# Performance work log

Measured on AMD Instinct MI355X. Metric: run time of the kernel, lower is better.

## Reference

```python
import jax, jax.numpy as jnp
import numpy as np

ROPE_BASE = 10000.0
NUM_HEADS = 16
NUM_KV_HEADS = 4


def _rms_norm(x, eps):
    # F.rms_norm with no weight: x / sqrt(mean(x^2) + eps)
    return x * jax.lax.rsqrt(jnp.mean(x * x, axis=-1, keepdims=True) + eps)


def _apply_rope(x, cos, sin):
    h = x.shape[-1] // 2
    x1, x2 = x[..., :h], x[..., h:]
    return jnp.concatenate([x1 * cos + x2 * sin, -x1 * sin + x2 * cos], axis=-1)


def setup_inputs() -> dict:
    key = jax.random.key(0)
    ks = jax.random.split(key, 5)
    B, T, D = 2, 2048, 1024
    H, Hkv = NUM_HEADS, NUM_KV_HEADS
    hd = D // H
    kv_dim = Hkv * hd
    s_in = 1.0 / np.sqrt(D)
    return {
        "x": jax.random.normal(ks[0], (B, T, D), dtype=jnp.float32),
        "Wq": jax.random.normal(ks[1], (D, D), dtype=jnp.float32) * s_in,
        "Wk": jax.random.normal(ks[2], (kv_dim, D), dtype=jnp.float32) * s_in,
        "Wv": jax.random.normal(ks[3], (kv_dim, D), dtype=jnp.float32) * s_in,
        "Wproj": jax.random.normal(ks[4], (D, D), dtype=jnp.float32) * s_in,
        "q_gain": jnp.full((H,), 1.0, dtype=jnp.float32),
    }


def reference(x, Wq, Wk, Wv, Wproj, q_gain):
    B, T, D = x.shape
    H, Hkv = NUM_HEADS, NUM_KV_HEADS
    hd = D // H
    rep = H // Hkv
    eps = jnp.finfo(x.dtype).eps

    # QKV projections (F.linear: x @ W.T)
    q = jnp.einsum('btd,od->bto', x, Wq).reshape(B, T, H, hd).transpose(0, 2, 1, 3)
    k = jnp.einsum('btd,od->bto', x, Wk).reshape(B, T, Hkv, hd).transpose(0, 2, 1, 3)
    v = jnp.einsum('btd,od->bto', x, Wv).reshape(B, T, Hkv, hd).transpose(0, 2, 1, 3)

    q = _rms_norm(q, eps)
    k = _rms_norm(k, eps)

    # RoPE tables: [1, 1, T, hd/2]
    inv_freq = 1.0 / (ROPE_BASE ** (jnp.arange(0, hd, 2, dtype=jnp.float32) / hd))
    f = jnp.arange(T, dtype=jnp.float32)[:, None] * inv_freq[None, :]
    cos = jnp.cos(f)[None, None].astype(q.dtype)
    sin = jnp.sin(f)[None, None].astype(q.dtype)
    q = _apply_rope(q, cos, sin)
    k = _apply_rope(k, cos, sin)

    q = q * q_gain.astype(q.dtype)[None, :, None, None]

    # GQA without materializing repeated K/V: group q heads [Hkv, rep]
    qg = q.reshape(B, Hkv, rep, T, hd)
    scale = hd ** -0.5
    scores = jnp.einsum('bgrqd,bgkd->bgrqk', qg, k) * scale
    causal = jnp.tril(jnp.ones((T, T), dtype=bool))
    scores = jnp.where(causal, scores, -jnp.inf)
    att = jax.nn.softmax(scores.astype(jnp.float32), axis=-1).astype(q.dtype)
    y = jnp.einsum('bgrqk,bgkd->bgrqd', att, v)  # [B,Hkv,rep,T,hd]
    y = y.reshape(B, H, T, hd).transpose(0, 2, 1, 3).reshape(B, T, D)
    return jnp.einsum('btd,od->bto', y, Wproj)
```

## Files before the change

### kernel.cpp

```cpp
#include <hip/hip_runtime.h>
#include <cstdint>
#include <cstddef>

typedef __attribute__((ext_vector_type(8))) short short8;
typedef __attribute__((ext_vector_type(4))) float floatx4;
typedef __attribute__((ext_vector_type(16))) float floatx16;
typedef __attribute__((ext_vector_type(4))) short short4v;
typedef unsigned short u16;
typedef unsigned int u32;

#define B_   2
#define T_   2048
#define D_   1024
#define H_   16
#define HKV_ 4
#define HD_  64
#define KV_  256
#define M_   4096
#define QS_  1536

#define NX   4194304
#define NWQ  1048576
#define NWK  262144
#define NWV  262144
#define NWP  1048576
#define NCAST (NX + NWQ + NWK + NWV + NWP)
#define CAST_BLOCKS (NCAST / 1024)
#define TAB_BLOCKS  256

__device__ __forceinline__ float b2f(u16 u) {
    union { u32 i; float f; } v; v.i = ((u32)u) << 16; return v.f;
}
__device__ __forceinline__ u16 f2b(float f) {
    union { float f; u32 i; } v; v.f = f;
    u32 r = v.i + 0x7FFF + ((v.i >> 16) & 1);
    return (u16)(r >> 16);
}

__device__ __forceinline__ void async16(const u16* g, u16* l) {
    __builtin_amdgcn_global_load_lds(
        (const __attribute__((address_space(1))) u32*)g,
        (__attribute__((address_space(3))) u32*)l, 16, 0, 0);
}

__device__ __forceinline__ u32 cvtpk(float lo, float hi) {
    u32 r;
    asm("v_cvt_pk_bf16_f32 %0, %1, %2" : "=v"(r) : "v"(lo), "v"(hi));
    return r;
}
__device__ __forceinline__ void swap32(u32& a, u32& b) {
    asm volatile("v_permlane32_swap_b32 %0, %1" : "+v"(a), "+v"(b));
}
__device__ __forceinline__ void swap32f(float& a, float& b) {
    asm volatile("v_permlane32_swap_b32 %0, %1" : "+v"(a), "+v"(b));
}
__device__ __forceinline__ short8 pkfrag(u32 w0, u32 w1, u32 w2, u32 w3) {
    union { u32 w[4]; short8 s; } u;
    u.w[0] = w0; u.w[1] = w1; u.w[2] = w2; u.w[3] = w3;
    return u.s;
}

__global__ __launch_bounds__(256) void prep(const float* __restrict__ x,
                                            const float* __restrict__ wq,
                                            const float* __restrict__ wk,
                                            const float* __restrict__ wv,
                                            const float* __restrict__ wp,
                                            u16* __restrict__ dst,
                                            float2* __restrict__ tab) {
    int blk = blockIdx.x;
    if (blk < CAST_BLOCKS) {
        int i = blk * 1024 + threadIdx.x * 4;
        const float* src; int off;
        if      (i < NX)                  { src = x;  off = i; }
        else if (i < NX+NWQ)              { src = wq; off = i - NX; }
        else if (i < NX+NWQ+NWK)          { src = wk; off = i - (NX+NWQ); }
        else if (i < NX+NWQ+NWK+NWV)      { src = wv; off = i - (NX+NWQ+NWK); }
        else                              { src = wp; off = i - (NX+NWQ+NWK+NWV); }
        float4 v = *(const float4*)(src + off);
        short4v o;
        o.x = (short)f2b(v.x); o.y = (short)f2b(v.y);
        o.z = (short)f2b(v.z); o.w = (short)f2b(v.w);
        *(short4v*)(dst + i) = o;
    } else {
        int idx = (blk - CAST_BLOCKS) * 256 + threadIdx.x;
        int t = idx >> 5, i = idx & 31;
        float freq = exp2f(-(float)i * (13.287712379549449f / 32.0f));
        float ang = (float)t * freq;
        tab[idx] = make_float2(cosf(ang), sinf(ang));
    }
}

__global__ __launch_bounds__(256, 3) void gemm_qkv(const u16* __restrict__ A,
                                                   const u16* __restrict__ W,
                                                   u16* __restrict__ C,
                                                   u16* __restrict__ Vt,
                                                   const float* __restrict__ gain,
                                                   const float2* __restrict__ tab) {
    const int K = D_;
    __shared__ u16 As[2][2][128 * 32];
    __shared__ u16 Bs[2][2][64 * 32];
    const int t = threadIdx.x;
    const int wave = t >> 6, lane = t & 63;
    const int quad = lane >> 4, l16 = lane & 15;
    const int wm = wave * 32;
    const int m0 = blockIdx.y * 128, n0 = blockIdx.x * 64;

    floatx4 acc[2][4];
#pragma unroll
    for (int i = 0; i < 2; i++)
#pragma unroll
        for (int j = 0; j < 4; j++) acc[i][j] = (floatx4){0.f, 0.f, 0.f, 0.f};

    const int sr = t >> 2;
    const int sc = (((t & 3) ^ ((t >> 3) & 3)) * 8);
    const u16* ga = A + (size_t)(m0 + sr) * K + sc;
    const u16* gb = W + (size_t)(n0 + sr) * K + sc;

    auto stage = [&](int buf, int half, int koff) {
        async16(ga + koff, As[buf][half] + t * 8);
        async16(ga + koff + (size_t)64 * K, As[buf][half] + t * 8 + 64 * 32);
        async16(gb + koff, Bs[buf][half] + t * 8);
    };

    stage(0, 0, 0);
    stage(0, 1, 32);

    int cur = 0;
    for (int kt = 0; kt < K; kt += 64) {
        __syncthreads();
        if (kt + 64 < K) {
            stage(cur ^ 1, 0, kt + 64);
            stage(cur ^ 1, 1, kt + 96);
        }
#pragma unroll
        for (int half = 0; half < 2; half++) {
            short8 af[2], bf[4];
#pragma unroll
            for (int mt = 0; mt < 2; mt++) {
                int row = wm + mt * 16 + l16;
                af[mt] = *(const short8*)(As[cur][half] + row * 32 +
                                          ((quad ^ ((row >> 1) & 3)) << 3));
            }
#pragma unroll
            for (int nt = 0; nt < 4; nt++) {
                int row = nt * 16 + l16;
                bf[nt] = *(const short8*)(Bs[cur][half] + row * 32 +
                                          ((quad ^ ((row >> 1) & 3)) << 3));
            }
#pragma unroll
            for (int mt = 0; mt < 2; mt++)
#pragma unroll
                for (int nt = 0; nt < 4; nt++)
                    acc[mt][nt] = __builtin_amdgcn_mfma_f32_16x16x32_bf16(
                        af[mt], bf[nt], acc[mt][nt], 0, 0, 0);
        }
        cur ^= 1;
    }

    const int col0 = n0;
    if (col0 < 1280) {
        float gs = (col0 < 1024)
                 ? gain[col0 >> 6] * (0.125f * 1.4426950408889634f)
                 : 1.0f;
#pragma unroll
        for (int mt = 0; mt < 2; mt++)
#pragma unroll
            for (int r = 0; r < 4; r++) {
                int row = m0 + wm + mt * 16 + quad * 4 + r;
                int tt = row & (T_ - 1);
                float v0 = acc[mt][0][r], v1 = acc[mt][1][r];
                float v2 = acc[mt][2][r], v3 = acc[mt][3][r];
                float ss = v0 * v0 + v1 * v1 + v2 * v2 + v3 * v3;
                ss += __shfl_xor(ss, 1); ss += __shfl_xor(ss, 2);
                ss += __shfl_xor(ss, 4); ss += __shfl_xor(ss, 8);
                float inv = rsqrtf(ss * (1.0f / 64.0f) + 1.1920929e-7f);
                v0 *= inv; v1 *= inv; v2 *= inv; v3 *= inv;
                float2 cs0 = tab[tt * 32 + l16];
                float2 cs1 = tab[tt * 32 + 16 + l16];
                float o0 = (v0 * cs0.x + v2 * cs0.y) * gs;
                float o1 = (v1 * cs1.x + v3 * cs1.y) * gs;
                float o2 = (v2 * cs0.x - v0 * cs0.y) * gs;
                float o3 = (v3 * cs1.x - v1 * cs1.y) * gs;
                u16* cp = C + (size_t)row * QS_ + col0 + l16;
                cp[0]  = f2b(o0);
                cp[16] = f2b(o1);
                cp[32] = f2b(o2);
                cp[48] = f2b(o3);
            }
    } else {
        const int g = (col0 - 1280) >> 6;
#pragma unroll
        for (int mt = 0; mt < 2; mt++)
#pragma unroll
            for (int r = 0; r < 4; r++) {
                int row = m0 + wm + mt * 16 + quad * 4 + r;
                int tt = row & (T_ - 1);
                int bb = row >> 11;
#pragma unroll
                for (int nt = 0; nt < 4; nt++)
                    Vt[(size_t)((bb * 4 + g) * 64 + nt * 16 + l16) * T_ + tt] =
                        f2b(acc[mt][nt][r]);
            }
    }
}

__global__ __launch_bounds__(256, 3) void gemm_proj(const u16* __restrict__ A,
                                                    const u16* __restrict__ W,
                                                    float* __restrict__ C) {
    const int K = D_;
    __shared__ u16 As[2][2][128 * 32];
    __shared__ u16 Bs[2][2][64 * 32];
    const int t = threadIdx.x;
    const int wave = t >> 6, lane = t & 63;
    const int quad = lane >> 4, l16 = lane & 15;
    const int wm = wave * 32;
    const int m0 = blockIdx.y * 128, n0 = blockIdx.x * 64;

    floatx4 acc[2][4];
#pragma unroll
    for (int i = 0; i < 2; i++)
#pragma unroll
        for (int j = 0; j < 4; j++) acc[i][j] = (floatx4){0.f, 0.f, 0.f, 0.f};

    const int sr = t >> 2;
    const int sc = (((t & 3) ^ ((t >> 3) & 3)) * 8);
    const u16* ga = A + (size_t)(m0 + sr) * K + sc;
    const u16* gb = W + (size_t)(n0 + sr) * K + sc;

    auto stage = [&](int buf, int half, int koff) {
        async16(ga + koff, As[buf][half] + t * 8);
        async16(ga + koff + (size_t)64 * K, As[buf][half] + t * 8 + 64 * 32);
        async16(gb + koff, Bs[buf][half] + t * 8);
    };

    stage(0, 0, 0);
    stage(0, 1, 32);

    int cur = 0;
    for (int kt = 0; kt < K; kt += 64) {
        __syncthreads();
        if (kt + 64 < K) {
            stage(cur ^ 1, 0, kt + 64);
            stage(cur ^ 1, 1, kt + 96);
        }
#pragma unroll
        for (int half = 0; half < 2; half++) {
            short8 af[2], bf[4];
#pragma unroll
            for (int mt = 0; mt < 2; mt++) {
                int row = wm + mt * 16 + l16;
                af[mt] = *(const short8*)(As[cur][half] + row * 32 +
                                          ((quad ^ ((row >> 1) & 3)) << 3));
            }
#pragma unroll
            for (int nt = 0; nt < 4; nt++) {
                int row = nt * 16 + l16;
                bf[nt] = *(const short8*)(Bs[cur][half] + row * 32 +
                                          ((quad ^ ((row >> 1) & 3)) << 3));
            }
#pragma unroll
            for (int mt = 0; mt < 2; mt++)
#pragma unroll
                for (int nt = 0; nt < 4; nt++)
                    acc[mt][nt] = __builtin_amdgcn_mfma_f32_16x16x32_bf16(
                        af[mt], bf[nt], acc[mt][nt], 0, 0, 0);
        }
        cur ^= 1;
    }

#pragma unroll
    for (int mt = 0; mt < 2; mt++)
#pragma unroll
        for (int nt = 0; nt < 4; nt++)
#pragma unroll
            for (int r = 0; r < 4; r++) {
                int row = m0 + wm + mt * 16 + quad * 4 + r;
                int col = n0 + nt * 16 + l16;
                C[(size_t)row * D_ + col] = acc[mt][nt][r];
            }
}

__global__ __launch_bounds__(256, 2) void flash(const u16* __restrict__ QKV,
                                                const u16* __restrict__ Vtr,
                                                u16* __restrict__ Y,
                                                float* __restrict__ Opart,
                                                float* __restrict__ Lpart) {
    const int u  = blockIdx.x;
    const int h  = blockIdx.y;
    const int b  = blockIdx.z;
    const int g  = h >> 2;
    const int w    = threadIdx.x >> 6;
    const int lane = threadIdx.x & 63;
    const int ln31 = lane & 31;
    const int hi   = lane >> 5;
    const int swz  = lane & 7;

    __shared__ u16 Kb[3][4096];
    __shared__ u16 Vb[3][4096];
    __shared__ float Ot[4][2048];

    const int srow = w * 16 + (lane >> 3);
    const int sseg = (lane & 7) ^ ((lane >> 3) & 7);
    const u16* kgb = QKV + (size_t)(b * T_ + srow) * QS_ + D_ + g * 64 + sseg * 8;
    const u16* vgb = Vtr + (size_t)((b * 4 + g) * 64 + srow) * T_ + sseg * 8;

    auto stage = [&](int tile, int bi) {
        const u16* kg = kgb + (size_t)tile * 64 * QS_;
        const u16* vg = vgb + (size_t)tile * 64;
        u16* kl = &Kb[bi][w * 1024 + lane * 8];
        u16* vl = &Vb[bi][w * 1024 + lane * 8];
        async16(kg, kl);
        async16(kg + (size_t)8 * QS_, kl + 512);
        async16(vg, vl);
        async16(vg + (size_t)8 * T_, vl + 512);
    };
    const bool low = (u < 8);
    auto tileOf = [&](int gidx) {
        return (low && gidx > 2 * u + 1) ? gidx + 15 - 2 * u : gidx;
    };

    stage(tileOf(0), 0);
    stage(tileOf(1), 1);

    const int nseg = low ? 2 : 1;
    const int buf  = low ? 0 : 1;
    int gi = 0;
    for (int seg = 0; seg < nseg; ++seg) {
        const int jt   = (low && seg == 0) ? u : (low ? 15 - u : u);
        const int nIt  = (low && seg == 0) ? 2 * u + 2 : (low ? 15 - 2 * u : 17);
        const bool direct = low && (seg == 0);
        const int qrow = jt * 128 + w * 32 + ln31;

        const u16* qp = QKV + (size_t)(b * T_ + qrow) * QS_ + h * HD_;
        short8 aq[4];
#pragma unroll
        for (int kc = 0; kc < 4; kc++)
            aq[kc] = *(const short8*)(qp + kc * 16 + hi * 8);

        floatx16 acc[2];
#pragma unroll
        for (int dh = 0; dh < 2; dh++)
#pragma unroll
            for (int i = 0; i < 16; i++) acc[dh][i] = 0.f;
        float l = 0.f;

        for (int itn = 0; itn < nIt; ++itn, ++gi) {
            const int tk = tileOf(gi);
            if (gi == 16) asm volatile("s_waitcnt vmcnt(0)" ::: "memory");
            else          asm volatile("s_waitcnt vmcnt(4)" ::: "memory");
            __builtin_amdgcn_s_barrier();
            asm volatile("" ::: "memory");

            const int bc = gi % 3;
            if (gi + 2 <= 16) stage(tileOf(gi + 2), (gi + 2) % 3);

            const u16* Kp = &Kb[bc][0];
            const u16* Vp = &Vb[bc][0];
            short8 kf[2][4], vfr[2][4];
#pragma unroll
            for (int kh = 0; kh < 2; kh++)
#pragma unroll
                for (int kc = 0; kc < 4; kc++)
                    kf[kh][kc] = *(const short8*)(Kp + (kh * 32 + ln31) * 64 +
                                                  (((kc * 2 + hi) ^ swz) << 3));
#pragma unroll
            for (int dh = 0; dh < 2; dh++)
#pragma unroll
                for (int kc = 0; kc < 4; kc++)
                    vfr[dh][kc] = *(const short8*)(Vp + (dh * 32 + ln31) * 64 +
                                                   (((kc * 2 + hi) ^ swz) << 3));

            floatx16 s[2];
#pragma unroll
            for (int kh = 0; kh < 2; kh++)
#pragma unroll
                for (int i = 0; i < 16; i++) s[kh][i] = 0.f;

            __builtin_amdgcn_s_setprio(1);
#pragma unroll
            for (int kc = 0; kc < 4; kc++) {
                s[0] = __builtin_amdgcn_mfma_f32_32x32x16_bf16(kf[0][kc], aq[kc], s[0], 0, 0, 0);
                s[1] = __builtin_amdgcn_mfma_f32_32x32x16_bf16(kf[1][kc], aq[kc], s[1], 0, 0, 0);
            }
            __builtin_amdgcn_s_setprio(0);

            u32 pw[2][8];
            if (tk >= 2 * jt) {
#pragma unroll
                for (int kh = 0; kh < 2; kh++)
#pragma unroll
                    for (int i = 0; i < 8; i++) {
                        int key0 = tk * 64 + kh * 32 +
                                   ((2 * i) & 3) + (((2 * i) >> 2) << 3) + (hi << 2);
                        float e0 = __builtin_amdgcn_exp2f(s[kh][2 * i]);
                        float e1 = __builtin_amdgcn_exp2f(s[kh][2 * i + 1]);
                        e0 = (key0 <= qrow) ? e0 : 0.f;
                        e1 = (key0 + 1 <= qrow) ? e1 : 0.f;
                        l += e0 + e1;
                        pw[kh][i] = cvtpk(e0, e1);
                    }
            } else {
#pragma unroll
                for (int kh = 0; kh < 2; kh++)
#pragma unroll
                    for (int i = 0; i < 8; i++) {
                        float e0 = __builtin_amdgcn_exp2f(s[kh][2 * i]);
                        float e1 = __builtin_amdgcn_exp2f(s[kh][2 * i + 1]);
                        l += e0 + e1;
                        pw[kh][i] = cvtpk(e0, e1);
                    }
            }

            short8 pb[4];
#pragma unroll
            for (int kh = 0; kh < 2; kh++) {
                u32 a0 = pw[kh][0], b0 = pw[kh][2], c0 = pw[kh][1], d0 = pw[kh][3];
                swap32(a0, b0); swap32(c0, d0);
                pb[kh * 2] = pkfrag(a0, c0, b0, d0);
                u32 a1 = pw[kh][4], b1 = pw[kh][6], c1 = pw[kh][5], d1 = pw[kh][7];
                swap32(a1, b1); swap32(c1, d1);
                pb[kh * 2 + 1] = pkfrag(a1, c1, b1, d1);
            }

            __builtin_amdgcn_s_setprio(1);
#pragma unroll
            for (int kc = 0; kc < 4; kc++) {
                acc[0] = __builtin_amdgcn_mfma_f32_32x32x16_bf16(vfr[0][kc], pb[kc], acc[0], 0, 0, 0);
                acc[1] = __builtin_amdgcn_mfma_f32_32x32x16_bf16(vfr[1][kc], pb[kc], acc[1], 0, 0, 0);
            }
            __builtin_amdgcn_s_setprio(0);
        }

        float la = l, lb = l;
        swap32f(la, lb);
        float lt = la + lb;

        if (direct) {
            float inv = 1.0f / lt;
#pragma unroll
            for (int dh = 0; dh < 2; dh++)
#pragma unroll
                for (int i = 0; i < 16; i++) acc[dh][i] *= inv;
        }

        float* ot = &Ot[w][0];
#pragma unroll
        for (int dh = 0; dh < 2; dh++)
#pragma unroll
            for (int g4 = 0; g4 < 4; g4++) {
                int ss = (dh * 8 + g4 * 2 + hi) ^ (ln31 & 7);
                float4 v = make_float4(acc[dh][g4 * 4 + 0], acc[dh][g4 * 4 + 1],
                                       acc[dh][g4 * 4 + 2], acc[dh][g4 * 4 + 3]);
                *(float4*)(ot + ln31 * 64 + ss * 4) = v;
            }
        asm volatile("s_waitcnt lgkmcnt(0)" ::: "memory");

        const int hq = lane >> 4;
        const int s4 = lane & 15;
        if (direct) {
            u16* ybase = Y + (size_t)(b * T_ + jt * 128 + w * 32) * D_ + h * HD_;
#pragma unroll
            for (int it = 0; it < 8; it++) {
                int q2 = it * 4 + hq;
                int ss = s4 ^ (q2 & 7);
                float4 v = *(const float4*)(ot + q2 * 64 + ss * 4);
                uint2 yw;
                yw.x = cvtpk(v.x, v.y);
                yw.y = cvtpk(v.z, v.w);
                *(uint2*)(ybase + (size_t)q2 * D_ + s4 * 4) = yw;
            }
        } else {
            const int rp = jt * 128 + w * 32 - 1024;
            float* obase = Opart + ((size_t)((buf * 2 + b) * 1024 + rp)) * 1024
                         + h * HD_;
#pragma unroll
            for (int it = 0; it < 8; it++) {
                int q2 = it * 4 + hq;
                int ss = s4 ^ (q2 & 7);
                float4 v = *(const float4*)(ot + q2 * 64 + ss * 4);
                *(float4*)(obase + (size_t)q2 * 1024 + s4 * 4) = v;
            }
            if (hi == 0)
                Lpart[((size_t)((buf * 2 + b) * 1024 + rp + ln31)) * 16 + h] = lt;
        }
    }
}

__global__ __launch_bounds__(256) void combine(const float* __restrict__ Opart,
                                               const float* __restrict__ Lpart,
                                               u16* __restrict__ Y) {
    int e = (blockIdx.x * 256 + threadIdx.x) * 4;
    int b = e >> 20;
    int rem = e & 1048575;
    int row = rem >> 10, col = rem & 1023;
    int li = (b * 1024 + row) * 16 + (col >> 6);
    float l0 = Lpart[li];
    float l1 = Lpart[li + 2 * 1024 * 16];
    float inv = 1.0f / (l0 + l1);
    size_t oi = ((size_t)(b * 1024 + row)) * 1024 + col;
    float4 o0 = *(const float4*)(Opart + oi);
    float4 o1 = *(const float4*)(Opart + oi + (size_t)2 * 1024 * 1024);
    short4v y;
    y.x = (short)f2b((o0.x + o1.x) * inv); y.y = (short)f2b((o0.y + o1.y) * inv);
    y.z = (short)f2b((o0.z + o1.z) * inv); y.w = (short)f2b((o0.w + o1.w) * inv);
    *(short4v*)(Y + (size_t)(b * T_ + 1024 + row) * D_ + col) = y;
}

extern "C" void kernel_launch(void* const* d_in, const int* in_sizes, int n_in,
                              void* d_out, int out_size, void* d_ws, size_t ws_size,
                              hipStream_t stream) {
    const float* x    = (const float*)d_in[0];
    const float* Wq   = (const float*)d_in[1];
    const float* Wk   = (const float*)d_in[2];
    const float* Wv   = (const float*)d_in[3];
    const float* Wp   = (const float*)d_in[4];
    const float* gain = (const float*)d_in[5];
    float* out = (float*)d_out;

    u16* xb   = (u16*)d_ws;
    u16* Wcat = xb + (size_t)NX;
    u16* Wpb  = Wcat + (size_t)(NWQ + NWK + NWV);
    u16* QKV  = Wpb + (size_t)NWP;
    u16* Vt   = QKV + (size_t)M_ * QS_;
    u16* Y    = Vt + (size_t)M_ * KV_;
    float2* tab = (float2*)(Y + (size_t)M_ * D_);
    float* Opart = (float*)(tab + 65536);
    float* Lpart = Opart + (size_t)4 * 1024 * 1024;

    prep<<<CAST_BLOCKS + TAB_BLOCKS, 256, 0, stream>>>(x, Wq, Wk, Wv, Wp, xb, tab);

    gemm_qkv<<<dim3(QS_ / 64, M_ / 128), 256, 0, stream>>>(xb, Wcat, QKV, Vt,
                                                           gain, tab);

    flash<<<dim3(16, H_, B_), 256, 0, stream>>>(QKV, Vt, Y, Opart, Lpart);

    combine<<<2048, 256, 0, stream>>>(Opart, Lpart, Y);

    gemm_proj<<<dim3(D_ / 64, M_ / 128), 256, 0, stream>>>(Y, Wpb, out);
}
```

Baseline: 160.4 us.

## Split flash warps 2x2 over query and key halves with LDS reduction

Restructures the flash kernel's warp work split. Each pair of warps now shares 64 query rows, and each warp handles one 32-key half of the K tile and one half of the V reduction dimension, instead of every warp owning 32 query rows against all 64 keys. This halves the K and V LDS fragment reads per warp and reuses each K fragment across two query blocks. In exchange it adds a cross-warp LDS reduction of the partial O and l, reusing a free V buffer for l, plus two extra barriers per segment, and it keeps more accumulator registers live.

```diff
diff --git a/kernel.cpp b/kernel.cpp
--- a/kernel.cpp
+++ b/kernel.cpp
@@ -294,10 +294,12 @@
     const int ln31 = lane & 31;
     const int hi   = lane >> 5;
     const int swz  = lane & 7;
+    const int qw   = w >> 1;
+    const int kw   = w & 1;
 
     __shared__ u16 Kb[3][4096];
     __shared__ u16 Vb[3][4096];
-    __shared__ float Ot[4][2048];
+    __shared__ float Ot[8192];
 
     const int srow = w * 16 + (lane >> 3);
     const int sseg = (lane & 7) ^ ((lane >> 3) & 7);
@@ -329,20 +331,25 @@
         const int jt   = (low && seg == 0) ? u : (low ? 15 - u : u);
         const int nIt  = (low && seg == 0) ? 2 * u + 2 : (low ? 15 - 2 * u : 17);
         const bool direct = low && (seg == 0);
-        const int qrow = jt * 128 + w * 32 + ln31;
-
-        const u16* qp = QKV + (size_t)(b * T_ + qrow) * QS_ + h * HD_;
-        short8 aq[4];
-#pragma unroll
-        for (int kc = 0; kc < 4; kc++)
-            aq[kc] = *(const short8*)(qp + kc * 16 + hi * 8);
-
-        floatx16 acc[2];
+        const int qbase = jt * 128 + qw * 64;
+
+        const u16* qp = QKV + (size_t)(b * T_ + qbase + ln31) * QS_ + h * HD_;
+        short8 aq[2][4];
+#pragma unroll
+        for (int qh = 0; qh < 2; qh++)
+#pragma unroll
+            for (int kc = 0; kc < 4; kc++)
+                aq[qh][kc] = *(const short8*)(qp + (size_t)qh * 32 * QS_ +
+                                              kc * 16 + hi * 8);
+
+        floatx16 acc[2][2];
 #pragma unroll
         for (int dh = 0; dh < 2; dh++)
 #pragma unroll
-            for (int i = 0; i < 16; i++) acc[dh][i] = 0.f;
-        float l = 0.f;
+            for (int qh = 0; qh < 2; qh++)
+#pragma unroll
+                for (int i = 0; i < 16; i++) acc[dh][qh][i] = 0.f;
+        float l[2] = {0.f, 0.f};
 
         for (int itn = 0; itn < nIt; ++itn, ++gi) {
             const int tk = tileOf(gi);
@@ -356,132 +363,201 @@
 
             const u16* Kp = &Kb[bc][0];
             const u16* Vp = &Vb[bc][0];
-            short8 kf[2][4], vfr[2][4];
-#pragma unroll
-            for (int kh = 0; kh < 2; kh++)
-#pragma unroll
-                for (int kc = 0; kc < 4; kc++)
-                    kf[kh][kc] = *(const short8*)(Kp + (kh * 32 + ln31) * 64 +
-                                                  (((kc * 2 + hi) ^ swz) << 3));
+
+            short8 kf[4];
+#pragma unroll
+            for (int kc = 0; kc < 4; kc++)
+                kf[kc] = *(const short8*)(Kp + (kw * 32 + ln31) * 64 +
+                                          (((kc * 2 + hi) ^ swz) << 3));
+
+            floatx16 s2[2];
+#pragma unroll
+            for (int qh = 0; qh < 2; qh++)
+#pragma unroll
+                for (int i = 0; i < 16; i++) s2[qh][i] = 0.f;
+
+            __builtin_amdgcn_s_setprio(1);
+#pragma unroll
+            for (int kc = 0; kc < 4; kc++) {
+                s2[0] = __builtin_amdgcn_mfma_f32_32x32x16_bf16(kf[kc], aq[0][kc], s2[0], 0, 0, 0);
+                s2[1] = __builtin_amdgcn_mfma_f32_32x32x16_bf16(kf[kc], aq[1][kc], s2[1], 0, 0, 0);
+            }
+            __builtin_amdgcn_s_setprio(0);
+
+            short8 vfr[2][2];
 #pragma unroll
             for (int dh = 0; dh < 2; dh++)
 #pragma unroll
-                for (int kc = 0; kc < 4; kc++)
-                    vfr[dh][kc] = *(const short8*)(Vp + (dh * 32 + ln31) * 64 +
-                                                   (((kc * 2 + hi) ^ swz) << 3));
-
-            floatx16 s[2];
-#pragma unroll
-            for (int kh = 0; kh < 2; kh++)
-#pragma unroll
-                for (int i = 0; i < 16; i++) s[kh][i] = 0.f;
-
-            __builtin_amdgcn_s_setprio(1);
-#pragma unroll
-            for (int kc = 0; kc < 4; kc++) {
-                s[0] = __builtin_amdgcn_mfma_f32_32x32x16_bf16(kf[0][kc], aq[kc], s[0], 0, 0, 0);
-                s[1] = __builtin_amdgcn_mfma_f32_32x32x16_bf16(kf[1][kc], aq[kc], s[1], 0, 0, 0);
-            }
-            __builtin_amdgcn_s_setprio(0);
-
-            u32 pw[2][8];
-            if (tk >= 2 * jt) {
-#pragma unroll
-                for (int kh = 0; kh < 2; kh++)
+                for (int kc2 = 0; kc2 < 2; kc2++)
+                    vfr[dh][kc2] = *(const short8*)(Vp + (dh * 32 + ln31) * 64 +
+                                        (((kw * 4 + kc2 * 2 + hi) ^ swz) << 3));
+
+            short8 pb[2][2];
+#pragma unroll
+            for (int qh = 0; qh < 2; qh++) {
+                const int qrow = qbase + qh * 32 + ln31;
+                u32 pw[8];
+                if (tk >= 2 * jt) {
 #pragma unroll
                     for (int i = 0; i < 8; i++) {
-                        int key0 = tk * 64 + kh * 32 +
+                        int key0 = tk * 64 + kw * 32 +
                                    ((2 * i) & 3) + (((2 * i) >> 2) << 3) + (hi << 2);
-                        float e0 = __builtin_amdgcn_exp2f(s[kh][2 * i]);
-                        float e1 = __builtin_amdgcn_exp2f(s[kh][2 * i + 1]);
+                        float e0 = __builtin_amdgcn_exp2f(s2[qh][2 * i]);
+                        float e1 = __builtin_amdgcn_exp2f(s2[qh][2 * i + 1]);
                         e0 = (key0 <= qrow) ? e0 : 0.f;
                         e1 = (key0 + 1 <= qrow) ? e1 : 0.f;
-                        l += e0 + e1;
-                        pw[kh][i] = cvtpk(e0, e1);
+                        l[qh] += e0 + e1;
+                        pw[i] = cvtpk(e0, e1);
                     }
-            } else {
-#pragma unroll
-                for (int kh = 0; kh < 2; kh++)
+                } else {
 #pragma unroll
                     for (int i = 0; i < 8; i++) {
-                        float e0 = __builtin_amdgcn_exp2f(s[kh][2 * i]);
-                        float e1 = __builtin_amdgcn_exp2f(s[kh][2 * i + 1]);
-                        l += e0 + e1;
-                        pw[kh][i] = cvtpk(e0, e1);
+                        float e0 = __builtin_amdgcn_exp2f(s2[qh][2 * i]);
+                        float e1 = __builtin_amdgcn_exp2f(s2[qh][2 * i + 1]);
+                        l[qh] += e0 + e1;
+                        pw[i] = cvtpk(e0, e1);
                     }
-            }
-
-            short8 pb[4];
-#pragma unroll
-            for (int kh = 0; kh < 2; kh++) {
-                u32 a0 = pw[kh][0], b0 = pw[kh][2], c0 = pw[kh][1], d0 = pw[kh][3];
+                }
+                u32 a0 = pw[0], c0 = pw[1], b0 = pw[2], d0 = pw[3];
                 swap32(a0, b0); swap32(c0, d0);
-                pb[kh * 2] = pkfrag(a0, c0, b0, d0);
-                u32 a1 = pw[kh][4], b1 = pw[kh][6], c1 = pw[kh][5], d1 = pw[kh][7];
+                pb[qh][0] = pkfrag(a0, c0, b0, d0);
+                u32 a1 = pw[4], c1 = pw[5], b1 = pw[6], d1 = pw[7];
                 swap32(a1, b1); swap32(c1, d1);
-                pb[kh * 2 + 1] = pkfrag(a1, c1, b1, d1);
+                pb[qh][1] = pkfrag(a1, c1, b1, d1);
             }
 
             __builtin_amdgcn_s_setprio(1);
 #pragma unroll
-            for (int kc = 0; kc < 4; kc++) {
-                acc[0] = __builtin_amdgcn_mfma_f32_32x32x16_bf16(vfr[0][kc], pb[kc], acc[0], 0, 0, 0);
-                acc[1] = __builtin_amdgcn_mfma_f32_32x32x16_bf16(vfr[1][kc], pb[kc], acc[1], 0, 0, 0);
+            for (int kc2 = 0; kc2 < 2; kc2++) {
+                acc[0][0] = __builtin_amdgcn_mfma_f32_32x32x16_bf16(vfr[0][kc2], pb[0][kc2], acc[0][0], 0, 0, 0);
+                acc[0][1] = __builtin_amdgcn_mfma_f32_32x32x16_bf16(vfr[0][kc2], pb[1][kc2], acc[0][1], 0, 0, 0);
+                acc[1][0] = __builtin_amdgcn_mfma_f32_32x32x16_bf16(vfr[1][kc2], pb[0][kc2], acc[1][0], 0, 0, 0);
+                acc[1][1] = __builtin_amdgcn_mfma_f32_32x32x16_bf16(vfr[1][kc2], pb[1][kc2], acc[1][1], 0, 0, 0);
             }
             __builtin_amdgcn_s_setprio(0);
         }
 
-        float la = l, lb = l;
-        swap32f(la, lb);
-        float lt = la + lb;
-
-        if (direct) {
-            float inv = 1.0f / lt;
+        float lt[2];
+#pragma unroll
+        for (int qh = 0; qh < 2; qh++) {
+            float la = l[qh], lb = l[qh];
+            swap32f(la, lb);
+            lt[qh] = la + lb;
+        }
+
+        const int fb = (gi + 2) % 3;
+        float* Lsh = (float*)&Vb[fb][0];
+        float* otq = Ot + qw * 4096;
+
+        __builtin_amdgcn_s_barrier();
+        asm volatile("" ::: "memory");
+
+        if (kw == 1) {
 #pragma unroll
             for (int dh = 0; dh < 2; dh++)
 #pragma unroll
-                for (int i = 0; i < 16; i++) acc[dh][i] *= inv;
-        }
-
-        float* ot = &Ot[w][0];
-#pragma unroll
-        for (int dh = 0; dh < 2; dh++)
-#pragma unroll
-            for (int g4 = 0; g4 < 4; g4++) {
-                int ss = (dh * 8 + g4 * 2 + hi) ^ (ln31 & 7);
-                float4 v = make_float4(acc[dh][g4 * 4 + 0], acc[dh][g4 * 4 + 1],
-                                       acc[dh][g4 * 4 + 2], acc[dh][g4 * 4 + 3]);
-                *(float4*)(ot + ln31 * 64 + ss * 4) = v;
-            }
+                for (int qh = 0; qh < 2; qh++)
+#pragma unroll
+                    for (int g4 = 0; g4 < 4; g4++) {
+                        int ql = qh * 32 + ln31;
+                        int ss = (dh * 8 + g4 * 2 + hi) ^ (ln31 & 7);
+                        float4 v = make_float4(acc[dh][qh][g4 * 4 + 0],
+                                               acc[dh][qh][g4 * 4 + 1],
+                                               acc[dh][qh][g4 * 4 + 2],
+                                               acc[dh][qh][g4 * 4 + 3]);
+                        *(float4*)(otq + ql * 64 + ss * 4) = v;
+                    }
+            if (hi == 0) {
+                Lsh[(qw * 2 + 0) * 32 + ln31] = lt[0];
+                Lsh[(qw * 2 + 1) * 32 + ln31] = lt[1];
+            }
+        }
         asm volatile("s_waitcnt lgkmcnt(0)" ::: "memory");
+        __builtin_amdgcn_s_barrier();
+        asm volatile("" ::: "memory");
+
+        if (kw == 0) {
+            float ltot[2];
+#pragma unroll
+            for (int qh = 0; qh < 2; qh++)
+                ltot[qh] = lt[qh] + Lsh[(qw * 2 + qh) * 32 + ln31];
+#pragma unroll
+            for (int dh = 0; dh < 2; dh++)
+#pragma unroll
+                for (int qh = 0; qh < 2; qh++)
+#pragma unroll
+                    for (int g4 = 0; g4 < 4; g4++) {
+                        int ql = qh * 32 + ln31;
+                        int ss = (dh * 8 + g4 * 2 + hi) ^ (ln31 & 7);
+                        float4 v = *(const float4*)(otq + ql * 64 + ss * 4);
+                        acc[dh][qh][g4 * 4 + 0] += v.x;
+                        acc[dh][qh][g4 * 4 + 1] += v.y;
+                        acc[dh][qh][g4 * 4 + 2] += v.z;
+                        acc[dh][qh][g4 * 4 + 3] += v.w;
+                    }
+            if (direct) {
+#pragma unroll
+                for (int qh = 0; qh < 2; qh++) {
+                    float inv = 1.0f / ltot[qh];
+#pragma unroll
+                    for (int dh = 0; dh < 2; dh++)
+#pragma unroll
+                        for (int i = 0; i < 16; i++) acc[dh][qh][i] *= inv;
+                }
+            }
+#pragma unroll
+            for (int dh = 0; dh < 2; dh++)
+#pragma unroll
+                for (int qh = 0; qh < 2; qh++)
+#pragma unroll
+                    for (int g4 = 0; g4 < 4; g4++) {
+                        int ql = qh * 32 + ln31;
+                        int ss = (dh * 8 + g4 * 2 + hi) ^ (ln31 & 7);
+                        float4 v = make_float4(acc[dh][qh][g4 * 4 + 0],
+                                               acc[dh][qh][g4 * 4 + 1],
+                                               acc[dh][qh][g4 * 4 + 2],
+                                               acc[dh][qh][g4 * 4 + 3]);
+                        *(float4*)(otq + ql * 64 + ss * 4) = v;
+                    }
+            if (!direct && hi == 0) {
+                int rbase = (buf * 2 + b) * 1024 + jt * 128 - 1024 + qw * 64;
+                Lpart[(size_t)(rbase + ln31) * 16 + h] = ltot[0];
+                Lpart[(size_t)(rbase + 32 + ln31) * 16 + h] = ltot[1];
+            }
+        }
+        asm volatile("s_waitcnt lgkmcnt(0)" ::: "memory");
+        __builtin_amdgcn_s_barrier();
+        asm volatile("" ::: "memory");
 
         const int hq = lane >> 4;
         const int s4 = lane & 15;
         if (direct) {
-            u16* ybase = Y + (size_t)(b * T_ + jt * 128 + w * 32) * D_ + h * HD_;
+            u16* ybase = Y + (size_t)(b * T_ + jt * 128) * D_ + h * HD_;
 #pragma unroll
             for (int it = 0; it < 8; it++) {
                 int q2 = it * 4 + hq;
+                int q128 = w * 32 + q2;
                 int ss = s4 ^ (q2 & 7);
-                float4 v = *(const float4*)(ot + q2 * 64 + ss * 4);
+                float4 v = *(const float4*)(Ot + (q128 >> 6) * 4096 +
+                                            (q128 & 63) * 64 + ss * 4);
                 uint2 yw;
                 yw.x = cvtpk(v.x, v.y);
                 yw.y = cvtpk(v.z, v.w);
-                *(uint2*)(ybase + (size_t)q2 * D_ + s4 * 4) = yw;
+                *(uint2*)(ybase + (size_t)q128 * D_ + s4 * 4) = yw;
             }
         } else {
-            const int rp = jt * 128 + w * 32 - 1024;
+            const int rp = jt * 128 - 1024;
             float* obase = Opart + ((size_t)((buf * 2 + b) * 1024 + rp)) * 1024
                          + h * HD_;
 #pragma unroll
             for (int it = 0; it < 8; it++) {
                 int q2 = it * 4 + hq;
+                int q128 = w * 32 + q2;
                 int ss = s4 ^ (q2 & 7);
-                float4 v = *(const float4*)(ot + q2 * 64 + ss * 4);
-                *(float4*)(obase + (size_t)q2 * 1024 + s4 * 4) = v;
-            }
-            if (hi == 0)
-                Lpart[((size_t)((buf * 2 + b) * 1024 + rp + ln31)) * 16 + h] = lt;
+                float4 v = *(const float4*)(Ot + (q128 >> 6) * 4096 +
+                                            (q128 & 63) * 64 + ss * 4);
+                *(float4*)(obase + (size_t)q128 * 1024 + s4 * 4) = v;
+            }
         }
     }
 }
```

Measured after the change: 160.6 us. About the same (+0.1%).

## Split key tiles across wave pairs in flash and drop combine kernel

Applied to the files above, without the earlier changes.

Flash attention now runs 512-thread blocks where each pair of waves shares a 32-row query tile and splits each 64-key tile in half, reducing partial outputs through shared memory. Each block handles a paired low/high query tile with the full key range, so the split-K global partials and the separate combine kernel are removed. This cuts a kernel launch and the fp32 partial-output traffic, at the cost of half as many blocks, extra barriers and an in-block reduction.

```diff
diff --git a/kernel.cpp b/kernel.cpp
--- a/kernel.cpp
+++ b/kernel.cpp
@@ -280,56 +280,47 @@
             }
 }
 
-__global__ __launch_bounds__(256, 2) void flash(const u16* __restrict__ QKV,
+__global__ __launch_bounds__(512, 1) void flash(const u16* __restrict__ QKV,
                                                 const u16* __restrict__ Vtr,
-                                                u16* __restrict__ Y,
-                                                float* __restrict__ Opart,
-                                                float* __restrict__ Lpart) {
+                                                u16* __restrict__ Y) {
     const int u  = blockIdx.x;
     const int h  = blockIdx.y;
     const int b  = blockIdx.z;
     const int g  = h >> 2;
-    const int w    = threadIdx.x >> 6;
-    const int lane = threadIdx.x & 63;
+    const int t  = threadIdx.x;
+    const int w    = t >> 6;
+    const int lane = t & 63;
     const int ln31 = lane & 31;
     const int hi   = lane >> 5;
     const int swz  = lane & 7;
+    const int qw   = w >> 1;
+    const int kw   = w & 1;
 
     __shared__ u16 Kb[3][4096];
     __shared__ u16 Vb[3][4096];
-    __shared__ float Ot[4][2048];
-
-    const int srow = w * 16 + (lane >> 3);
-    const int sseg = (lane & 7) ^ ((lane >> 3) & 7);
+    __shared__ float Ot[8192];
+
+    const int srow = t >> 3;
+    const int sseg = (t & 7) ^ (srow & 7);
     const u16* kgb = QKV + (size_t)(b * T_ + srow) * QS_ + D_ + g * 64 + sseg * 8;
     const u16* vgb = Vtr + (size_t)((b * 4 + g) * 64 + srow) * T_ + sseg * 8;
 
     auto stage = [&](int tile, int bi) {
-        const u16* kg = kgb + (size_t)tile * 64 * QS_;
-        const u16* vg = vgb + (size_t)tile * 64;
-        u16* kl = &Kb[bi][w * 1024 + lane * 8];
-        u16* vl = &Vb[bi][w * 1024 + lane * 8];
-        async16(kg, kl);
-        async16(kg + (size_t)8 * QS_, kl + 512);
-        async16(vg, vl);
-        async16(vg + (size_t)8 * T_, vl + 512);
+        async16(kgb + (size_t)tile * 64 * QS_, &Kb[bi][t * 8]);
+        async16(vgb + (size_t)tile * 64,       &Vb[bi][t * 8]);
     };
-    const bool low = (u < 8);
-    auto tileOf = [&](int gidx) {
-        return (low && gidx > 2 * u + 1) ? gidx + 15 - 2 * u : gidx;
-    };
+    const int n0 = 2 * u + 2;
+    auto tileOf = [&](int gidx) { return (gidx < n0) ? gidx : gidx - n0; };
 
     stage(tileOf(0), 0);
     stage(tileOf(1), 1);
 
-    const int nseg = low ? 2 : 1;
-    const int buf  = low ? 0 : 1;
     int gi = 0;
-    for (int seg = 0; seg < nseg; ++seg) {
-        const int jt   = (low && seg == 0) ? u : (low ? 15 - u : u);
-        const int nIt  = (low && seg == 0) ? 2 * u + 2 : (low ? 15 - 2 * u : 17);
-        const bool direct = low && (seg == 0);
-        const int qrow = jt * 128 + w * 32 + ln31;
+    for (int seg = 0; seg < 2; ++seg) {
+        const int jt  = seg ? 15 - u : u;
+        const int nIt = seg ? 32 - 2 * u : 2 * u + 2;
+        const int qbase = jt * 128 + qw * 32;
+        const int qrow  = qbase + ln31;
 
         const u16* qp = QKV + (size_t)(b * T_ + qrow) * QS_ + h * HD_;
         short8 aq[4];
@@ -346,88 +337,76 @@
 
         for (int itn = 0; itn < nIt; ++itn, ++gi) {
             const int tk = tileOf(gi);
-            if (gi == 16) asm volatile("s_waitcnt vmcnt(0)" ::: "memory");
-            else          asm volatile("s_waitcnt vmcnt(4)" ::: "memory");
+            if (gi == 33) asm volatile("s_waitcnt vmcnt(0)" ::: "memory");
+            else          asm volatile("s_waitcnt vmcnt(2)" ::: "memory");
             __builtin_amdgcn_s_barrier();
             asm volatile("" ::: "memory");
 
             const int bc = gi % 3;
-            if (gi + 2 <= 16) stage(tileOf(gi + 2), (gi + 2) % 3);
+            if (gi + 2 <= 33) stage(tileOf(gi + 2), (gi + 2) % 3);
 
             const u16* Kp = &Kb[bc][0];
             const u16* Vp = &Vb[bc][0];
-            short8 kf[2][4], vfr[2][4];
-#pragma unroll
-            for (int kh = 0; kh < 2; kh++)
-#pragma unroll
-                for (int kc = 0; kc < 4; kc++)
-                    kf[kh][kc] = *(const short8*)(Kp + (kh * 32 + ln31) * 64 +
-                                                  (((kc * 2 + hi) ^ swz) << 3));
+
+            short8 kf[4];
+#pragma unroll
+            for (int kc = 0; kc < 4; kc++)
+                kf[kc] = *(const short8*)(Kp + (kw * 32 + ln31) * 64 +
+                                          (((kc * 2 + hi) ^ swz) << 3));
+
+            floatx16 s2;
+#pragma unroll
+            for (int i = 0; i < 16; i++) s2[i] = 0.f;
+
+            __builtin_amdgcn_s_setprio(1);
+#pragma unroll
+            for (int kc = 0; kc < 4; kc++)
+                s2 = __builtin_amdgcn_mfma_f32_32x32x16_bf16(kf[kc], aq[kc], s2, 0, 0, 0);
+            __builtin_amdgcn_s_setprio(0);
+
+            short8 vfr[2][2];
 #pragma unroll
             for (int dh = 0; dh < 2; dh++)
 #pragma unroll
-                for (int kc = 0; kc < 4; kc++)
-                    vfr[dh][kc] = *(const short8*)(Vp + (dh * 32 + ln31) * 64 +
-                                                   (((kc * 2 + hi) ^ swz) << 3));
-
-            floatx16 s[2];
-#pragma unroll
-            for (int kh = 0; kh < 2; kh++)
-#pragma unroll
-                for (int i = 0; i < 16; i++) s[kh][i] = 0.f;
+                for (int kc2 = 0; kc2 < 2; kc2++)
+                    vfr[dh][kc2] = *(const short8*)(Vp + (dh * 32 + ln31) * 64 +
+                                        (((kw * 4 + kc2 * 2 + hi) ^ swz) << 3));
+
+            u32 pw[8];
+            if (tk >= 2 * jt) {
+#pragma unroll
+                for (int i = 0; i < 8; i++) {
+                    int key0 = tk * 64 + kw * 32 +
+                               ((2 * i) & 3) + (((2 * i) >> 2) << 3) + (hi << 2);
+                    float e0 = __builtin_amdgcn_exp2f(s2[2 * i]);
+                    float e1 = __builtin_amdgcn_exp2f(s2[2 * i + 1]);
+                    e0 = (key0 <= qrow) ? e0 : 0.f;
+                    e1 = (key0 + 1 <= qrow) ? e1 : 0.f;
+                    l += e0 + e1;
+                    pw[i] = cvtpk(e0, e1);
+                }
+            } else {
+#pragma unroll
+                for (int i = 0; i < 8; i++) {
+                    float e0 = __builtin_amdgcn_exp2f(s2[2 * i]);
+                    float e1 = __builtin_amdgcn_exp2f(s2[2 * i + 1]);
+                    l += e0 + e1;
+                    pw[i] = cvtpk(e0, e1);
+                }
+            }
+
+            u32 a0 = pw[0], c0 = pw[1], b0 = pw[2], d0 = pw[3];
+            swap32(a0, b0); swap32(c0, d0);
+            short8 pb0 = pkfrag(a0, c0, b0, d0);
+            u32 a1 = pw[4], c1 = pw[5], b1 = pw[6], d1 = pw[7];
+            swap32(a1, b1); swap32(c1, d1);
+            short8 pb1 = pkfrag(a1, c1, b1, d1);
 
             __builtin_amdgcn_s_setprio(1);
-#pragma unroll
-            for (int kc = 0; kc < 4; kc++) {
-                s[0] = __builtin_amdgcn_mfma_f32_32x32x16_bf16(kf[0][kc], aq[kc], s[0], 0, 0, 0);
-                s[1] = __builtin_amdgcn_mfma_f32_32x32x16_bf16(kf[1][kc], aq[kc], s[1], 0, 0, 0);
-            }
-            __builtin_amdgcn_s_setprio(0);
-
-            u32 pw[2][8];
-            if (tk >= 2 * jt) {
-#pragma unroll
-                for (int kh = 0; kh < 2; kh++)
-#pragma unroll
-                    for (int i = 0; i < 8; i++) {
-                        int key0 = tk * 64 + kh * 32 +
-                                   ((2 * i) & 3) + (((2 * i) >> 2) << 3) + (hi << 2);
-                        float e0 = __builtin_amdgcn_exp2f(s[kh][2 * i]);
-                        float e1 = __builtin_amdgcn_exp2f(s[kh][2 * i + 1]);
-                        e0 = (key0 <= qrow) ? e0 : 0.f;
-                        e1 = (key0 + 1 <= qrow) ? e1 : 0.f;
-                        l += e0 + e1;
-                        pw[kh][i] = cvtpk(e0, e1);
-                    }
-            } else {
-#pragma unroll
-                for (int kh = 0; kh < 2; kh++)
-#pragma unroll
-                    for (int i = 0; i < 8; i++) {
-                        float e0 = __builtin_amdgcn_exp2f(s[kh][2 * i]);
-                        float e1 = __builtin_amdgcn_exp2f(s[kh][2 * i + 1]);
-                        l += e0 + e1;
-                        pw[kh][i] = cvtpk(e0, e1);
-                    }
-            }
-
-            short8 pb[4];
-#pragma unroll
-            for (int kh = 0; kh < 2; kh++) {
-                u32 a0 = pw[kh][0], b0 = pw[kh][2], c0 = pw[kh][1], d0 = pw[kh][3];
-                swap32(a0, b0); swap32(c0, d0);
-                pb[kh * 2] = pkfrag(a0, c0, b0, d0);
-                u32 a1 = pw[kh][4], b1 = pw[kh][6], c1 = pw[kh][5], d1 = pw[kh][7];
-                swap32(a1, b1); swap32(c1, d1);
-                pb[kh * 2 + 1] = pkfrag(a1, c1, b1, d1);
-            }
-
-            __builtin_amdgcn_s_setprio(1);
-#pragma unroll
-            for (int kc = 0; kc < 4; kc++) {
-                acc[0] = __builtin_amdgcn_mfma_f32_32x32x16_bf16(vfr[0][kc], pb[kc], acc[0], 0, 0, 0);
-                acc[1] = __builtin_amdgcn_mfma_f32_32x32x16_bf16(vfr[1][kc], pb[kc], acc[1], 0, 0, 0);
-            }
+            acc[0] = __builtin_amdgcn_mfma_f32_32x32x16_bf16(vfr[0][0], pb0, acc[0], 0, 0, 0);
+            acc[1] = __builtin_amdgcn_mfma_f32_32x32x16_bf16(vfr[1][0], pb0, acc[1], 0, 0, 0);
+            acc[0] = __builtin_amdgcn_mfma_f32_32x32x16_bf16(vfr[0][1], pb1, acc[0], 0, 0, 0);
+            acc[1] = __builtin_amdgcn_mfma_f32_32x32x16_bf16(vfr[1][1], pb1, acc[1], 0, 0, 0);
             __builtin_amdgcn_s_setprio(0);
         }
 
@@ -435,75 +414,67 @@
         swap32f(la, lb);
         float lt = la + lb;
 
-        if (direct) {
-            float inv = 1.0f / lt;
+        const int fb = (gi + 2) % 3;
+        float* Lsh = (float*)&Vb[fb][0];
+        float* otq = Ot + qw * 2048;
+
+        __builtin_amdgcn_s_barrier();
+        asm volatile("" ::: "memory");
+
+        if (kw == 1) {
 #pragma unroll
             for (int dh = 0; dh < 2; dh++)
 #pragma unroll
-                for (int i = 0; i < 16; i++) acc[dh][i] *= inv;
-        }
-
-        float* ot = &Ot[w][0];
-#pragma unroll
-        for (int dh = 0; dh < 2; dh++)
-#pragma unroll
-            for (int g4 = 0; g4 < 4; g4++) {
-                int ss = (dh * 8 + g4 * 2 + hi) ^ (ln31 & 7);
-                float4 v = make_float4(acc[dh][g4 * 4 + 0], acc[dh][g4 * 4 + 1],
-                                       acc[dh][g4 * 4 + 2], acc[dh][g4 * 4 + 3]);
-                *(float4*)(ot + ln31 * 64 + ss * 4) = v;
-            }
+                for (int g4 = 0; g4 < 4; g4++) {
+                    int ss = (dh * 8 + g4 * 2 + hi) ^ (ln31 & 7);
+                    float4 v = make_float4(acc[dh][g4 * 4 + 0],
+                                           acc[dh][g4 * 4 + 1],
+                                           acc[dh][g4 * 4 + 2],
+                                           acc[dh][g4 * 4 + 3]);
+                    *(float4*)(otq + ln31 * 64 + ss * 4) = v;
+                }
+            if (hi == 0) Lsh[qw * 32 + ln31] = lt;
+        }
         asm volatile("s_waitcnt lgkmcnt(0)" ::: "memory");
+        __builtin_amdgcn_s_barrier();
+        asm volatile("" ::: "memory");
+
+        if (kw == 0) {
+            float ltot = lt + Lsh[qw * 32 + ln31];
+            float inv = 1.0f / ltot;
+#pragma unroll
+            for (int dh = 0; dh < 2; dh++)
+#pragma unroll
+                for (int g4 = 0; g4 < 4; g4++) {
+                    int ss = (dh * 8 + g4 * 2 + hi) ^ (ln31 & 7);
+                    float4 v = *(const float4*)(otq + ln31 * 64 + ss * 4);
+                    float4 o;
+                    o.x = (acc[dh][g4 * 4 + 0] + v.x) * inv;
+                    o.y = (acc[dh][g4 * 4 + 1] + v.y) * inv;
+                    o.z = (acc[dh][g4 * 4 + 2] + v.z) * inv;
+                    o.w = (acc[dh][g4 * 4 + 3] + v.w) * inv;
+                    *(float4*)(otq + ln31 * 64 + ss * 4) = o;
+                }
+        }
+        asm volatile("s_waitcnt lgkmcnt(0)" ::: "memory");
+        __builtin_amdgcn_s_barrier();
+        asm volatile("" ::: "memory");
 
         const int hq = lane >> 4;
         const int s4 = lane & 15;
-        if (direct) {
-            u16* ybase = Y + (size_t)(b * T_ + jt * 128 + w * 32) * D_ + h * HD_;
-#pragma unroll
-            for (int it = 0; it < 8; it++) {
-                int q2 = it * 4 + hq;
-                int ss = s4 ^ (q2 & 7);
-                float4 v = *(const float4*)(ot + q2 * 64 + ss * 4);
-                uint2 yw;
-                yw.x = cvtpk(v.x, v.y);
-                yw.y = cvtpk(v.z, v.w);
-                *(uint2*)(ybase + (size_t)q2 * D_ + s4 * 4) = yw;
-            }
-        } else {
-            const int rp = jt * 128 + w * 32 - 1024;
-            float* obase = Opart + ((size_t)((buf * 2 + b) * 1024 + rp)) * 1024
-                         + h * HD_;
-#pragma unroll
-            for (int it = 0; it < 8; it++) {
-                int q2 = it * 4 + hq;
-                int ss = s4 ^ (q2 & 7);
-                float4 v = *(const float4*)(ot + q2 * 64 + ss * 4);
-                *(float4*)(obase + (size_t)q2 * 1024 + s4 * 4) = v;
-            }
-            if (hi == 0)
-                Lpart[((size_t)((buf * 2 + b) * 1024 + rp + ln31)) * 16 + h] = lt;
+        u16* ybase = Y + (size_t)(b * T_ + jt * 128) * D_ + h * HD_;
+#pragma unroll
+        for (int it = 0; it < 4; it++) {
+            int q128 = w * 16 + it * 4 + hq;
+            int ql = q128 & 31, rg = q128 >> 5;
+            int ss = s4 ^ (ql & 7);
+            float4 v = *(const float4*)(Ot + rg * 2048 + ql * 64 + ss * 4);
+            uint2 yw;
+            yw.x = cvtpk(v.x, v.y);
+            yw.y = cvtpk(v.z, v.w);
+            *(uint2*)(ybase + (size_t)q128 * D_ + s4 * 4) = yw;
         }
     }
-}
-
-__global__ __launch_bounds__(256) void combine(const float* __restrict__ Opart,
-                                               const float* __restrict__ Lpart,
-                                               u16* __restrict__ Y) {
-    int e = (blockIdx.x * 256 + threadIdx.x) * 4;
-    int b = e >> 20;
-    int rem = e & 1048575;
-    int row = rem >> 10, col = rem & 1023;
-    int li = (b * 1024 + row) * 16 + (col >> 6);
-    float l0 = Lpart[li];
-    float l1 = Lpart[li + 2 * 1024 * 16];
-    float inv = 1.0f / (l0 + l1);
-    size_t oi = ((size_t)(b * 1024 + row)) * 1024 + col;
-    float4 o0 = *(const float4*)(Opart + oi);
-    float4 o1 = *(const float4*)(Opart + oi + (size_t)2 * 1024 * 1024);
-    short4v y;
-    y.x = (short)f2b((o0.x + o1.x) * inv); y.y = (short)f2b((o0.y + o1.y) * inv);
-    y.z = (short)f2b((o0.z + o1.z) * inv); y.w = (short)f2b((o0.w + o1.w) * inv);
-    *(short4v*)(Y + (size_t)(b * T_ + 1024 + row) * D_ + col) = y;
 }
 
 extern "C" void kernel_launch(void* const* d_in, const int* in_sizes, int n_in,
@@ -524,17 +495,13 @@
     u16* Vt   = QKV + (size_t)M_ * QS_;
     u16* Y    = Vt + (size_t)M_ * KV_;
     float2* tab = (float2*)(Y + (size_t)M_ * D_);
-    float* Opart = (float*)(tab + 65536);
-    float* Lpart = Opart + (size_t)4 * 1024 * 1024;
 
     prep<<<CAST_BLOCKS + TAB_BLOCKS, 256, 0, stream>>>(x, Wq, Wk, Wv, Wp, xb, tab);
 
     gemm_qkv<<<dim3(QS_ / 64, M_ / 128), 256, 0, stream>>>(xb, Wcat, QKV, Vt,
                                                            gain, tab);
 
-    flash<<<dim3(16, H_, B_), 256, 0, stream>>>(QKV, Vt, Y, Opart, Lpart);
-
-    combine<<<2048, 256, 0, stream>>>(Opart, Lpart, Y);
+    flash<<<dim3(8, H_, B_), 512, 0, stream>>>(QKV, Vt, Y);
 
     gemm_proj<<<dim3(D_ / 64, M_ / 128), 256, 0, stream>>>(Y, Wpb, out);
 }
```

Result: slower. 163.7 us (+2.1%).
